# Performance work log

Hardware: AMD Instinct MI355X
Metric: run time of the kernel (lower is better)

Reference implementation:

```python
import jax, jax.numpy as jnp
import numpy as np

B = 65536
IN1, IN2 = 384, 128
GRU1, GRU2, NLEVELS = 384, 16, 256


def gru_step(x, h, kernel, rkernel, bias):
    """Single Keras GRU (reset_after=True) step. Gate order: z, r, h.
    kernel: [in, 3u], rkernel: [u, 3u], bias: [2, 3u] (input bias, recurrent bias)."""
    u = h.shape[-1]
    xi = x @ kernel + bias[0]          # [B, 3u]
    hr = h @ rkernel + bias[1]         # [B, 3u]
    xz, xr, xh = xi[:, :u], xi[:, u:2 * u], xi[:, 2 * u:]
    hz, hrr, hh = hr[:, :u], hr[:, u:2 * u], hr[:, 2 * u:]
    z = jax.nn.sigmoid(xz + hz)
    r = jax.nn.sigmoid(xr + hrr)
    hcand = jnp.tanh(xh + r * hh)
    return z * h + (1.0 - z) * hcand


def setup_inputs() -> dict:
    key = jax.random.key(0)
    ks = jax.random.split(key, 14)
    s = lambda fan: 1.0 / np.sqrt(fan)
    return {
        "x1": jax.random.normal(ks[0], (B, IN1), jnp.float32),
        "x2": jax.random.normal(ks[1], (B, IN2), jnp.float32),
        "gru1_kernel": jax.random.normal(ks[2], (IN1 + IN2, 3 * GRU1), jnp.float32) * s(IN1 + IN2),
        "gru1_rkernel": jax.random.normal(ks[3], (GRU1, 3 * GRU1), jnp.float32) * s(GRU1),
        "gru1_bias": jax.random.normal(ks[4], (2, 3 * GRU1), jnp.float32) * 0.01,
        "gru2_kernel": jax.random.normal(ks[5], (GRU1, 3 * GRU2), jnp.float32) * s(GRU1),
        "gru2_rkernel": jax.random.normal(ks[6], (GRU2, 3 * GRU2), jnp.float32) * s(GRU2),
        "gru2_bias": jax.random.normal(ks[7], (2, 3 * GRU2), jnp.float32) * 0.01,
        "fc_w1": jax.random.normal(ks[8], (GRU2, NLEVELS), jnp.float32) * s(GRU2),
        "fc_b1": jax.random.normal(ks[9], (NLEVELS,), jnp.float32) * 0.01,
        "fc_w2": jax.random.normal(ks[10], (GRU2, NLEVELS), jnp.float32) * s(GRU2),
        "fc_b2": jax.random.normal(ks[11], (NLEVELS,), jnp.float32) * 0.01,
        "fc_g1": jax.random.normal(ks[12], (NLEVELS,), jnp.float32),
        "fc_g2": jax.random.normal(ks[13], (NLEVELS,), jnp.float32),
    }


def reference(x1, x2, gru1_kernel, gru1_rkernel, gru1_bias,
              gru2_kernel, gru2_rkernel, gru2_bias,
              fc_w1, fc_b1, fc_w2, fc_b2, fc_g1, fc_g2):
    e = jnp.concatenate([x1, x2], axis=-1)                      # [B, 512]
    h1 = gru_step(e, jnp.zeros((e.shape[0], GRU1), e.dtype),
                  gru1_kernel, gru1_rkernel, gru1_bias)         # [B, 384]
    h2 = gru_step(h1, jnp.zeros((e.shape[0], GRU2), e.dtype),
                  gru2_kernel, gru2_rkernel, gru2_bias)         # [B, 16]
    # DualFC (LPCNet): weighted sum of two tanh branches
    d = fc_g1 * jnp.tanh(h2 @ fc_w1 + fc_b1) + fc_g2 * jnp.tanh(h2 @ fc_w2 + fc_b2)
    return jax.nn.softmax(d, axis=-1)                           # [B, 256]
```

## Files before the change

### kernel.cpp

```cpp
#include <hip/hip_runtime.h>

typedef unsigned short u16;
typedef unsigned int   u32;
typedef float f32x4 __attribute__((ext_vector_type(4)));
typedef short s16x8 __attribute__((ext_vector_type(8)));

#define NB    65536
#define K1    512
#define N1    1152
#define G1D   384
#define K2    384
#define G2D   16
#define NL    256

__device__ inline u16 f2bf(float f) {
  u32 u = __float_as_uint(f);
  u += 0x7fffu + ((u >> 16) & 1u);
  return (u16)(u >> 16);
}
__device__ inline float bf2f(u16 h) { return __uint_as_float(((u32)h) << 16); }
__device__ inline float sigmoidf_(float x) { return 1.0f / (1.0f + __expf(-x)); }
__device__ inline float tanhf_(float x) {
  float e = __expf(2.0f * fabsf(x));
  float t = 1.0f - 2.0f / (e + 1.0f);
  return copysignf(t, x);
}

__device__ inline void gld16(const u16* g, u16* l) {
  __builtin_amdgcn_global_load_lds(
      (const __attribute__((address_space(1))) void*)g,
      (__attribute__((address_space(3))) void*)l, 16, 0, 0);
}

__global__ void prep_a(const float* __restrict__ x1, const float* __restrict__ x2,
                       u16* __restrict__ Abf) {
  int t = blockIdx.x * 256 + threadIdx.x;
  int i = t * 8;
  int row = i >> 9, col = i & 511;
  const float* src = (col < 384) ? (x1 + row * 384 + col) : (x2 + row * 128 + (col - 384));
  float4 v0 = ((const float4*)src)[0];
  float4 v1 = ((const float4*)src)[1];
  union { uint4 v; u16 u[8]; } o;
  o.u[0] = f2bf(v0.x); o.u[1] = f2bf(v0.y); o.u[2] = f2bf(v0.z); o.u[3] = f2bf(v0.w);
  o.u[4] = f2bf(v1.x); o.u[5] = f2bf(v1.y); o.u[6] = f2bf(v1.z); o.u[7] = f2bf(v1.w);
  *(uint4*)(Abf + i) = o.v;
}

__global__ __launch_bounds__(256) void prep_wt1(const float* __restrict__ w,
                                                u16* __restrict__ wt) {
  __shared__ float tile[64][65];
  const int nt = blockIdx.x * 64;
  const int ktb = blockIdx.y * 64;
  const int tr = threadIdx.x >> 4;
  const int tc = (threadIdx.x & 15) * 4;
#pragma unroll
  for (int p = 0; p < 4; p++) {
    int k = ktb + p * 16 + tr;
    float4 v = *(const float4*)(w + (long)k * N1 + nt + tc);
    tile[p * 16 + tr][tc + 0] = v.x;
    tile[p * 16 + tr][tc + 1] = v.y;
    tile[p * 16 + tr][tc + 2] = v.z;
    tile[p * 16 + tr][tc + 3] = v.w;
  }
  __syncthreads();
  const int nl = threadIdx.x >> 3;
  const int kc = (threadIdx.x & 7) * 8;
#pragma unroll
  for (int p = 0; p < 2; p++) {
    int n = nl + p * 32;
    int c = nt + n;
    int g = c / 384;
    int urem = c - g * 384;
    int ut = urem >> 4, u16c = urem & 15;
    int k0 = ktb + kc;
    int kt = k0 >> 5, qd = (k0 >> 3) & 3;
    union { uint4 v; u16 u[8]; } o;
#pragma unroll
    for (int j = 0; j < 8; j++) o.u[j] = f2bf(tile[kc + j][n]);
    long off = ((long)((g * 24 + ut) * 16 + kt) * 64 + qd * 16 + u16c) * 8;
    *(uint4*)(wt + off) = o.v;
  }
}

__global__ void prep_wt(const float* __restrict__ w, u16* __restrict__ wt, int K, int N) {
  int n = blockIdx.x;
  int k0 = threadIdx.x * 8;
  if (k0 >= K) return;
  union { uint4 v; u16 u[8]; } o;
#pragma unroll
  for (int j = 0; j < 8; j++) o.u[j] = f2bf(w[(k0 + j) * N + n]);
  *(uint4*)(wt + n * K + k0) = o.v;
}

__global__ __launch_bounds__(256, 2) void gemm1gate(const u16* __restrict__ A,
                                                    const u16* __restrict__ Bf,
                                                    const float* __restrict__ bias,
                                                    u16* __restrict__ H1) {
  __shared__ u16 As[4][128 * 32];
  const int tid = threadIdx.x;
  const int wave = tid >> 6, lane = tid & 63;
  const int quad = lane >> 4, l16 = lane & 15;

  const int id = blockIdx.x;
  const int xcd = id & 7;
  const int s = id >> 3;
  const int sd6 = s / 6;
  const int ublk = s - sd6 * 6;
  const int mbase = (xcd * 64 + sd6) * 128;
  const int ucbase = ublk * 64;

  const int wm = (wave & 1) * 64, wu = (wave >> 1) * 32;
  const int ut0 = ublk * 4 + (wave >> 1) * 2;

  f32x4 acc[3][4][2];
#pragma unroll
  for (int g = 0; g < 3; g++)
#pragma unroll
    for (int i = 0; i < 4; i++)
#pragma unroll
      for (int j = 0; j < 2; j++)
#pragma unroll
        for (int r = 0; r < 4; r++) acc[g][i][j][r] = 0.0f;

  const int r0 = tid >> 2;
  const int kcg = ((tid & 3) ^ ((r0 >> 1) & 3)) * 8;
  const u16* Aptr  = A + (long)(mbase + r0) * K1 + kcg;
  const u16* Aptr2 = Aptr + 64 * K1;
  const u16* Bl = Bf + lane * 8;

  int aoff[4];
#pragma unroll
  for (int i = 0; i < 4; i++) {
    int ra = wm + i * 16 + l16;
    aoff[i] = ra * 32 + ((quad ^ ((ra >> 1) & 3)) << 3);
  }

  s16x8 bn[3][2];
#pragma unroll
  for (int g = 0; g < 3; g++)
#pragma unroll
    for (int j = 0; j < 2; j++)
      bn[g][j] = *(const s16x8*)(Bl + (long)((g * 24 + ut0 + j) * 16 + 0) * 512);
  asm volatile("" ::: "memory");
  gld16(Aptr,       &As[0][tid * 8]);
  gld16(Aptr2,      &As[0][2048 + tid * 8]);
  gld16(Aptr + 32,  &As[1][tid * 8]);
  gld16(Aptr2 + 32, &As[1][2048 + tid * 8]);

#pragma unroll
  for (int t = 0; t < 16; ++t) {
    s16x8 bcur[3][2];
#pragma unroll
    for (int g = 0; g < 3; g++)
#pragma unroll
      for (int j = 0; j < 2; j++) bcur[g][j] = bn[g][j];

    if (t < 15) {
      const int tb = t + 1;
#pragma unroll
      for (int g = 0; g < 3; g++)
#pragma unroll
        for (int j = 0; j < 2; j++)
          bn[g][j] = *(const s16x8*)(Bl + (long)((g * 24 + ut0 + j) * 16 + tb) * 512);
    }
    asm volatile("" ::: "memory");
    if (t < 14) {
      const int ta = t + 2;
      gld16(Aptr  + ta * 32, &As[(t + 2) & 3][tid * 8]);
      gld16(Aptr2 + ta * 32, &As[(t + 2) & 3][2048 + tid * 8]);
    }
    if (t == 0)       asm volatile("s_waitcnt vmcnt(10)" ::: "memory");
    else if (t < 14)  asm volatile("s_waitcnt vmcnt(16)" ::: "memory");
    else if (t == 14) asm volatile("s_waitcnt vmcnt(14)" ::: "memory");
    else              asm volatile("s_waitcnt vmcnt(6)"  ::: "memory");
    __builtin_amdgcn_s_barrier();
    asm volatile("" ::: "memory");

    const u16* buf = &As[t & 3][0];
    s16x8 af[4];
#pragma unroll
    for (int i = 0; i < 4; i++) af[i] = *(const s16x8*)(buf + aoff[i]);

    __builtin_amdgcn_s_setprio(1);
#pragma unroll
    for (int g = 0; g < 3; g++) {
#pragma unroll
      for (int mi = 0; mi < 4; mi++) {
        acc[g][mi][0] = __builtin_amdgcn_mfma_f32_16x16x32_bf16(af[mi], bcur[g][0], acc[g][mi][0], 0, 0, 0);
        acc[g][mi][1] = __builtin_amdgcn_mfma_f32_16x16x32_bf16(af[mi], bcur[g][1], acc[g][mi][1], 0, 0, 0);
      }
    }
    __builtin_amdgcn_s_setprio(0);
  }

#pragma unroll
  for (int j = 0; j < 2; j++) {
    int u = ucbase + wu + j * 16 + l16;
    float bz = bias[u] + bias[1152 + u];
    float br = bias[384 + u] + bias[1536 + u];
    float bh0 = bias[768 + u];
    float bh1 = bias[1920 + u];
#pragma unroll
    for (int mi = 0; mi < 4; mi++) {
#pragma unroll
      for (int rr = 0; rr < 4; rr++) {
        int row = mbase + wm + mi * 16 + quad * 4 + rr;
        float z  = sigmoidf_(acc[0][mi][j][rr] + bz);
        float rg = sigmoidf_(acc[1][mi][j][rr] + br);
        float hc = tanhf_(acc[2][mi][j][rr] + bh0 + rg * bh1);
        H1[(long)row * G1D + u] = f2bf((1.0f - z) * hc);
      }
    }
  }
}

__global__ __launch_bounds__(256) void gemm2fc(const u16* __restrict__ H1b,
                                               const u16* __restrict__ W2t,
                                               const float* __restrict__ bias2,
                                               const float* __restrict__ w1,
                                               const float* __restrict__ fb1,
                                               const float* __restrict__ w2,
                                               const float* __restrict__ fb2,
                                               const float* __restrict__ g1,
                                               const float* __restrict__ g2,
                                               float* __restrict__ out) {
  __shared__ u16 As[128 * 32];
  __shared__ u16 Bs[48 * 32];
  __shared__ float h2s[128 * 17];
  const int tid = threadIdx.x;
  const int wave = tid >> 6, lane = tid & 63;
  const int quad = lane >> 4, l16 = lane & 15;
  const int mbase = blockIdx.x * 128;

  f32x4 acc[2][3];
#pragma unroll
  for (int i = 0; i < 2; i++)
#pragma unroll
    for (int j = 0; j < 3; j++)
#pragma unroll
      for (int r = 0; r < 4; r++) acc[i][j][r] = 0.0f;

  const int r0 = tid >> 2, kc = (tid & 3) * 8;
  const u16* Aptr = H1b + (long)(mbase + r0) * K2 + kc;

  for (int k0 = 0; k0 < K2; k0 += 32) {
    uint4 a0 = *(const uint4*)(Aptr + k0);
    uint4 a1 = *(const uint4*)(Aptr + 64 * K2 + k0);
    uint4 bv;
    if (tid < 192) bv = *(const uint4*)(W2t + r0 * K2 + k0 + kc);
    __syncthreads();
    *(uint4*)(&As[r0 * 32 + kc]) = a0;
    *(uint4*)(&As[(64 + r0) * 32 + kc]) = a1;
    if (tid < 192) *(uint4*)(&Bs[r0 * 32 + kc]) = bv;
    __syncthreads();
    s16x8 af[2], bfr[3];
#pragma unroll
    for (int mi = 0; mi < 2; mi++)
      af[mi] = *(const s16x8*)(&As[(wave * 32 + mi * 16 + l16) * 32 + quad * 8]);
#pragma unroll
    for (int ni = 0; ni < 3; ni++)
      bfr[ni] = *(const s16x8*)(&Bs[(ni * 16 + l16) * 32 + quad * 8]);
#pragma unroll
    for (int mi = 0; mi < 2; mi++)
#pragma unroll
      for (int ni = 0; ni < 3; ni++)
        acc[mi][ni] = __builtin_amdgcn_mfma_f32_16x16x32_bf16(af[mi], bfr[ni], acc[mi][ni], 0, 0, 0);
  }

  {
    const int u = l16;
    const float b0z = bias2[u],      b1z = bias2[48 + u];
    const float b0r = bias2[16 + u], b1r = bias2[64 + u];
    const float b0h = bias2[32 + u], b1h = bias2[80 + u];
#pragma unroll
    for (int mi = 0; mi < 2; mi++) {
#pragma unroll
      for (int rr = 0; rr < 4; rr++) {
        int row_l = wave * 32 + mi * 16 + quad * 4 + rr;
        float z  = sigmoidf_(acc[mi][0][rr] + b0z + b1z);
        float rg = sigmoidf_(acc[mi][1][rr] + b0r + b1r);
        float hc = tanhf_(acc[mi][2][rr] + b0h + rg * b1h);
        h2s[row_l * 17 + u] = (1.0f - z) * hc;
      }
    }
  }
  __syncthreads();

#pragma unroll 1
  for (int r = 0; r < 32; r++) {
    int row_l = wave * 32 + r;
    float h[16];
#pragma unroll
    for (int uu = 0; uu < 16; uu++) h[uu] = h2s[row_l * 17 + uu];
    float e[4];
    float mx = -1e30f;
#pragma unroll
    for (int i = 0; i < 4; i++) {
      int c = i * 64 + lane;
      float a1 = fb1[c], a2 = fb2[c];
#pragma unroll
      for (int uu = 0; uu < 16; uu++) {
        a1 = fmaf(h[uu], w1[uu * 256 + c], a1);
        a2 = fmaf(h[uu], w2[uu * 256 + c], a2);
      }
      float d = g1[c] * tanhf_(a1) + g2[c] * tanhf_(a2);
      e[i] = d;
      mx = fmaxf(mx, d);
    }
#pragma unroll
    for (int off = 32; off >= 1; off >>= 1) mx = fmaxf(mx, __shfl_xor(mx, off, 64));
    float sum = 0.0f;
#pragma unroll
    for (int i = 0; i < 4; i++) { e[i] = __expf(e[i] - mx); sum += e[i]; }
#pragma unroll
    for (int off = 32; off >= 1; off >>= 1) sum += __shfl_xor(sum, off, 64);
    float inv = 1.0f / sum;
    float* orow = out + (long)(mbase + row_l) * NL;
#pragma unroll
    for (int i = 0; i < 4; i++) orow[i * 64 + lane] = e[i] * inv;
  }
}

extern "C" void kernel_launch(void* const* d_in, const int* in_sizes, int n_in,
                              void* d_out, int out_size, void* d_ws, size_t ws_size,
                              hipStream_t stream) {
  const float* x1   = (const float*)d_in[0];
  const float* x2   = (const float*)d_in[1];
  const float* w1k  = (const float*)d_in[2];
  const float* b1g  = (const float*)d_in[4];
  const float* w2k  = (const float*)d_in[5];
  const float* b2g  = (const float*)d_in[7];
  const float* fcw1 = (const float*)d_in[8];
  const float* fcb1 = (const float*)d_in[9];
  const float* fcw2 = (const float*)d_in[10];
  const float* fcb2 = (const float*)d_in[11];
  const float* fcg1 = (const float*)d_in[12];
  const float* fcg2 = (const float*)d_in[13];
  float* out = (float*)d_out;

  char* ws = (char*)d_ws;
  u16* Abf = (u16*)(ws + 0);
  u16* W1t = (u16*)(ws + 67108864);
  u16* H1  = (u16*)(ws + 68288512);
  u16* W2t = (u16*)(ws + 118620160);

  hipLaunchKernelGGL(prep_a, dim3(16384), dim3(256), 0, stream, x1, x2, Abf);
  hipLaunchKernelGGL(prep_wt1, dim3(18, 8), dim3(256), 0, stream, w1k, W1t);
  hipLaunchKernelGGL(prep_wt, dim3(48), dim3(64), 0, stream, w2k, W2t, 384, 48);
  hipLaunchKernelGGL(gemm1gate, dim3(3072), dim3(256), 0, stream, Abf, W1t, b1g, H1);
  hipLaunchKernelGGL(gemm2fc, dim3(512), dim3(256), 0, stream, H1, W2t, b2g,
                     fcw1, fcb1, fcw2, fcb2, fcg1, fcg2, out);
}
```

Baseline: 364.9 us.

## Halve gemm1gate tile width to double occupancy and block count

```diff
diff --git a/kernel.cpp b/kernel.cpp
--- a/kernel.cpp
+++ b/kernel.cpp
@@ -92,7 +92,7 @@
   *(uint4*)(wt + n * K + k0) = o.v;
 }
 
-__global__ __launch_bounds__(256, 2) void gemm1gate(const u16* __restrict__ A,
+__global__ __launch_bounds__(256, 4) void gemm1gate(const u16* __restrict__ A,
                                                     const u16* __restrict__ Bf,
                                                     const float* __restrict__ bias,
                                                     u16* __restrict__ H1) {
@@ -104,23 +104,22 @@
   const int id = blockIdx.x;
   const int xcd = id & 7;
   const int s = id >> 3;
-  const int sd6 = s / 6;
-  const int ublk = s - sd6 * 6;
-  const int mbase = (xcd * 64 + sd6) * 128;
-  const int ucbase = ublk * 64;
-
-  const int wm = (wave & 1) * 64, wu = (wave >> 1) * 32;
-  const int ut0 = ublk * 4 + (wave >> 1) * 2;
-
-  f32x4 acc[3][4][2];
+  const int sd = s / 12;
+  const int ublk = s - sd * 12;
+  const int mbase = (xcd * 64 + sd) * 128;
+  const int ucbase = ublk * 32;
+
+  const int wm = (wave & 1) * 64;
+  const int wuidx = wave >> 1;
+  const int ut0 = ublk * 2 + wuidx;
+
+  f32x4 acc[3][4];
 #pragma unroll
   for (int g = 0; g < 3; g++)
 #pragma unroll
     for (int i = 0; i < 4; i++)
 #pragma unroll
-      for (int j = 0; j < 2; j++)
-#pragma unroll
-        for (int r = 0; r < 4; r++) acc[g][i][j][r] = 0.0f;
+      for (int r = 0; r < 4; r++) acc[g][i][r] = 0.0f;
 
   const int r0 = tid >> 2;
   const int kcg = ((tid & 3) ^ ((r0 >> 1) & 3)) * 8;
@@ -135,12 +134,10 @@
     aoff[i] = ra * 32 + ((quad ^ ((ra >> 1) & 3)) << 3);
   }
 
-  s16x8 bn[3][2];
+  s16x8 bn[3];
 #pragma unroll
   for (int g = 0; g < 3; g++)
-#pragma unroll
-    for (int j = 0; j < 2; j++)
-      bn[g][j] = *(const s16x8*)(Bl + (long)((g * 24 + ut0 + j) * 16 + 0) * 512);
+    bn[g] = *(const s16x8*)(Bl + (long)((g * 24 + ut0) * 16 + 0) * 512);
   asm volatile("" ::: "memory");
   gld16(Aptr,       &As[0][tid * 8]);
   gld16(Aptr2,      &As[0][2048 + tid * 8]);
@@ -149,19 +146,15 @@
 
 #pragma unroll
   for (int t = 0; t < 16; ++t) {
-    s16x8 bcur[3][2];
-#pragma unroll
-    for (int g = 0; g < 3; g++)
-#pragma unroll
-      for (int j = 0; j < 2; j++) bcur[g][j] = bn[g][j];
+    s16x8 bcur[3];
+#pragma unroll
+    for (int g = 0; g < 3; g++) bcur[g] = bn[g];
 
     if (t < 15) {
       const int tb = t + 1;
 #pragma unroll
       for (int g = 0; g < 3; g++)
-#pragma unroll
-        for (int j = 0; j < 2; j++)
-          bn[g][j] = *(const s16x8*)(Bl + (long)((g * 24 + ut0 + j) * 16 + tb) * 512);
+        bn[g] = *(const s16x8*)(Bl + (long)((g * 24 + ut0) * 16 + tb) * 512);
     }
     asm volatile("" ::: "memory");
     if (t < 14) {
@@ -169,10 +162,9 @@
       gld16(Aptr  + ta * 32, &As[(t + 2) & 3][tid * 8]);
       gld16(Aptr2 + ta * 32, &As[(t + 2) & 3][2048 + tid * 8]);
     }
-    if (t == 0)       asm volatile("s_waitcnt vmcnt(10)" ::: "memory");
-    else if (t < 14)  asm volatile("s_waitcnt vmcnt(16)" ::: "memory");
-    else if (t == 14) asm volatile("s_waitcnt vmcnt(14)" ::: "memory");
-    else              asm volatile("s_waitcnt vmcnt(6)"  ::: "memory");
+    if (t < 14)       asm volatile("s_waitcnt vmcnt(7)" ::: "memory");
+    else if (t == 14) asm volatile("s_waitcnt vmcnt(5)" ::: "memory");
+    else              asm volatile("s_waitcnt vmcnt(0)" ::: "memory");
     __builtin_amdgcn_s_barrier();
     asm volatile("" ::: "memory");
 
@@ -186,16 +178,14 @@
     for (int g = 0; g < 3; g++) {
 #pragma unroll
       for (int mi = 0; mi < 4; mi++) {
-        acc[g][mi][0] = __builtin_amdgcn_mfma_f32_16x16x32_bf16(af[mi], bcur[g][0], acc[g][mi][0], 0, 0, 0);
-        acc[g][mi][1] = __builtin_amdgcn_mfma_f32_16x16x32_bf16(af[mi], bcur[g][1], acc[g][mi][1], 0, 0, 0);
+        acc[g][mi] = __builtin_amdgcn_mfma_f32_16x16x32_bf16(af[mi], bcur[g], acc[g][mi], 0, 0, 0);
       }
     }
     __builtin_amdgcn_s_setprio(0);
   }
 
-#pragma unroll
-  for (int j = 0; j < 2; j++) {
-    int u = ucbase + wu + j * 16 + l16;
+  {
+    int u = ucbase + wuidx * 16 + l16;
     float bz = bias[u] + bias[1152 + u];
     float br = bias[384 + u] + bias[1536 + u];
     float bh0 = bias[768 + u];
@@ -205,9 +195,9 @@
 #pragma unroll
       for (int rr = 0; rr < 4; rr++) {
         int row = mbase + wm + mi * 16 + quad * 4 + rr;
-        float z  = sigmoidf_(acc[0][mi][j][rr] + bz);
-        float rg = sigmoidf_(acc[1][mi][j][rr] + br);
-        float hc = tanhf_(acc[2][mi][j][rr] + bh0 + rg * bh1);
+        float z  = sigmoidf_(acc[0][mi][rr] + bz);
+        float rg = sigmoidf_(acc[1][mi][rr] + br);
+        float hc = tanhf_(acc[2][mi][rr] + bh0 + rg * bh1);
         H1[(long)row * G1D + u] = f2bf((1.0f - z) * hc);
       }
     }
@@ -347,7 +337,7 @@
   hipLaunchKernelGGL(prep_a, dim3(16384), dim3(256), 0, stream, x1, x2, Abf);
   hipLaunchKernelGGL(prep_wt1, dim3(18, 8), dim3(256), 0, stream, w1k, W1t);
   hipLaunchKernelGGL(prep_wt, dim3(48), dim3(64), 0, stream, w2k, W2t, 384, 48);
-  hipLaunchKernelGGL(gemm1gate, dim3(3072), dim3(256), 0, stream, Abf, W1t, b1g, H1);
+  hipLaunchKernelGGL(gemm1gate, dim3(6144), dim3(256), 0, stream, Abf, W1t, b1g, H1);
   hipLaunchKernelGGL(gemm2fc, dim3(512), dim3(256), 0, stream, H1, W2t, b2g,
                      fcw1, fcb1, fcw2, fcb2, fcg1, fcg2, out);
 }
```

Result: slower. 373.2 us (+2.3%).

## Retile GRU1 GEMM to 256-row blocks and merge weight prep kernels

Applied to the files above, without the earlier changes.

```diff
diff --git a/kernel.cpp b/kernel.cpp
--- a/kernel.cpp
+++ b/kernel.cpp
@@ -46,57 +46,61 @@
   *(uint4*)(Abf + i) = o.v;
 }
 
-__global__ __launch_bounds__(256) void prep_wt1(const float* __restrict__ w,
-                                                u16* __restrict__ wt) {
+__global__ __launch_bounds__(256) void prep_w(const float* __restrict__ w1k,
+                                              u16* __restrict__ W1t,
+                                              const float* __restrict__ w2k,
+                                              u16* __restrict__ W2t) {
   __shared__ float tile[64][65];
-  const int nt = blockIdx.x * 64;
-  const int ktb = blockIdx.y * 64;
-  const int tr = threadIdx.x >> 4;
-  const int tc = (threadIdx.x & 15) * 4;
-#pragma unroll
-  for (int p = 0; p < 4; p++) {
-    int k = ktb + p * 16 + tr;
-    float4 v = *(const float4*)(w + (long)k * N1 + nt + tc);
-    tile[p * 16 + tr][tc + 0] = v.x;
-    tile[p * 16 + tr][tc + 1] = v.y;
-    tile[p * 16 + tr][tc + 2] = v.z;
-    tile[p * 16 + tr][tc + 3] = v.w;
-  }
-  __syncthreads();
-  const int nl = threadIdx.x >> 3;
-  const int kc = (threadIdx.x & 7) * 8;
-#pragma unroll
-  for (int p = 0; p < 2; p++) {
-    int n = nl + p * 32;
-    int c = nt + n;
-    int g = c / 384;
-    int urem = c - g * 384;
-    int ut = urem >> 4, u16c = urem & 15;
-    int k0 = ktb + kc;
-    int kt = k0 >> 5, qd = (k0 >> 3) & 3;
-    union { uint4 v; u16 u[8]; } o;
-#pragma unroll
-    for (int j = 0; j < 8; j++) o.u[j] = f2bf(tile[kc + j][n]);
-    long off = ((long)((g * 24 + ut) * 16 + kt) * 64 + qd * 16 + u16c) * 8;
-    *(uint4*)(wt + off) = o.v;
-  }
-}
-
-__global__ void prep_wt(const float* __restrict__ w, u16* __restrict__ wt, int K, int N) {
-  int n = blockIdx.x;
-  int k0 = threadIdx.x * 8;
-  if (k0 >= K) return;
-  union { uint4 v; u16 u[8]; } o;
-#pragma unroll
-  for (int j = 0; j < 8; j++) o.u[j] = f2bf(w[(k0 + j) * N + n]);
-  *(uint4*)(wt + n * K + k0) = o.v;
+  const int id = blockIdx.x;
+  if (id < 144) {
+    const int nt = (id % 18) * 64;
+    const int ktb = (id / 18) * 64;
+    const int tr = threadIdx.x >> 4;
+    const int tc = (threadIdx.x & 15) * 4;
+#pragma unroll
+    for (int p = 0; p < 4; p++) {
+      int k = ktb + p * 16 + tr;
+      float4 v = *(const float4*)(w1k + (long)k * N1 + nt + tc);
+      tile[p * 16 + tr][tc + 0] = v.x;
+      tile[p * 16 + tr][tc + 1] = v.y;
+      tile[p * 16 + tr][tc + 2] = v.z;
+      tile[p * 16 + tr][tc + 3] = v.w;
+    }
+    __syncthreads();
+    const int nl = threadIdx.x >> 3;
+    const int kc = (threadIdx.x & 7) * 8;
+#pragma unroll
+    for (int p = 0; p < 2; p++) {
+      int n = nl + p * 32;
+      int c = nt + n;
+      int g = c / 384;
+      int urem = c - g * 384;
+      int ut = urem >> 4, u16c = urem & 15;
+      int k0 = ktb + kc;
+      int kt = k0 >> 5, qd = (k0 >> 3) & 3;
+      union { uint4 v; u16 u[8]; } o;
+#pragma unroll
+      for (int j = 0; j < 8; j++) o.u[j] = f2bf(tile[kc + j][n]);
+      long off = ((long)((g * 24 + ut) * 16 + kt) * 64 + qd * 16 + u16c) * 8;
+      *(uint4*)(W1t + off) = o.v;
+    }
+  } else {
+    const int n = id - 144;
+    if (threadIdx.x < 48) {
+      const int k0 = threadIdx.x * 8;
+      union { uint4 v; u16 u[8]; } o;
+#pragma unroll
+      for (int j = 0; j < 8; j++) o.u[j] = f2bf(w2k[(k0 + j) * 48 + n]);
+      *(uint4*)(W2t + n * K2 + k0) = o.v;
+    }
+  }
 }
 
 __global__ __launch_bounds__(256, 2) void gemm1gate(const u16* __restrict__ A,
                                                     const u16* __restrict__ Bf,
                                                     const float* __restrict__ bias,
                                                     u16* __restrict__ H1) {
-  __shared__ u16 As[4][128 * 32];
+  __shared__ u16 As[4][256 * 32];
   const int tid = threadIdx.x;
   const int wave = tid >> 6, lane = tid & 63;
   const int quad = lane >> 4, l16 = lane & 15;
@@ -104,13 +108,12 @@
   const int id = blockIdx.x;
   const int xcd = id & 7;
   const int s = id >> 3;
-  const int sd6 = s / 6;
-  const int ublk = s - sd6 * 6;
-  const int mbase = (xcd * 64 + sd6) * 128;
-  const int ucbase = ublk * 64;
-
-  const int wm = (wave & 1) * 64, wu = (wave >> 1) * 32;
-  const int ut0 = ublk * 4 + (wave >> 1) * 2;
+  const int sd = s / 12;
+  const int ublk = s - sd * 12;
+  const int mbase = (xcd * 32 + sd) * 256;
+  const int ucbase = ublk * 32;
+  const int wm = wave * 64;
+  const int ut0 = ublk * 2;
 
   f32x4 acc[3][4][2];
 #pragma unroll
@@ -124,8 +127,10 @@
 
   const int r0 = tid >> 2;
   const int kcg = ((tid & 3) ^ ((r0 >> 1) & 3)) * 8;
-  const u16* Aptr  = A + (long)(mbase + r0) * K1 + kcg;
-  const u16* Aptr2 = Aptr + 64 * K1;
+  const u16* Ap0 = A + (long)(mbase + r0) * K1 + kcg;
+  const u16* Ap1 = Ap0 + 64 * K1;
+  const u16* Ap2 = Ap0 + 128 * K1;
+  const u16* Ap3 = Ap0 + 192 * K1;
   const u16* Bl = Bf + lane * 8;
 
   int aoff[4];
@@ -135,17 +140,27 @@
     aoff[i] = ra * 32 + ((quad ^ ((ra >> 1) & 3)) << 3);
   }
 
+#define BLOAD(T, DST) do {                                                   \
+    _Pragma("unroll")                                                        \
+    for (int g_ = 0; g_ < 3; g_++)                                           \
+      _Pragma("unroll")                                                      \
+      for (int j_ = 0; j_ < 2; j_++)                                         \
+        DST[g_][j_] = *(const s16x8*)(Bl +                                   \
+            (long)((g_ * 24 + ut0 + j_) * 16 + (T)) * 512);                  \
+  } while (0)
+
+#define STAGEA(T, BUFI) do {                                                 \
+    gld16(Ap0 + (T) * 32, &As[BUFI][0 * 2048 + tid * 8]);                    \
+    gld16(Ap1 + (T) * 32, &As[BUFI][1 * 2048 + tid * 8]);                    \
+    gld16(Ap2 + (T) * 32, &As[BUFI][2 * 2048 + tid * 8]);                    \
+    gld16(Ap3 + (T) * 32, &As[BUFI][3 * 2048 + tid * 8]);                    \
+  } while (0)
+
   s16x8 bn[3][2];
-#pragma unroll
-  for (int g = 0; g < 3; g++)
-#pragma unroll
-    for (int j = 0; j < 2; j++)
-      bn[g][j] = *(const s16x8*)(Bl + (long)((g * 24 + ut0 + j) * 16 + 0) * 512);
+  BLOAD(0, bn);
   asm volatile("" ::: "memory");
-  gld16(Aptr,       &As[0][tid * 8]);
-  gld16(Aptr2,      &As[0][2048 + tid * 8]);
-  gld16(Aptr + 32,  &As[1][tid * 8]);
-  gld16(Aptr2 + 32, &As[1][2048 + tid * 8]);
+  STAGEA(0, 0);
+  STAGEA(1, 1);
 
 #pragma unroll
   for (int t = 0; t < 16; ++t) {
@@ -155,24 +170,12 @@
 #pragma unroll
       for (int j = 0; j < 2; j++) bcur[g][j] = bn[g][j];
 
-    if (t < 15) {
-      const int tb = t + 1;
-#pragma unroll
-      for (int g = 0; g < 3; g++)
-#pragma unroll
-        for (int j = 0; j < 2; j++)
-          bn[g][j] = *(const s16x8*)(Bl + (long)((g * 24 + ut0 + j) * 16 + tb) * 512);
-    }
+    if (t < 15) BLOAD(t + 1, bn);
     asm volatile("" ::: "memory");
-    if (t < 14) {
-      const int ta = t + 2;
-      gld16(Aptr  + ta * 32, &As[(t + 2) & 3][tid * 8]);
-      gld16(Aptr2 + ta * 32, &As[(t + 2) & 3][2048 + tid * 8]);
-    }
-    if (t == 0)       asm volatile("s_waitcnt vmcnt(10)" ::: "memory");
-    else if (t < 14)  asm volatile("s_waitcnt vmcnt(16)" ::: "memory");
-    else if (t == 14) asm volatile("s_waitcnt vmcnt(14)" ::: "memory");
-    else              asm volatile("s_waitcnt vmcnt(6)"  ::: "memory");
+    if (t < 14) STAGEA(t + 2, (t + 2) & 3);
+    if (t < 14)       asm volatile("s_waitcnt vmcnt(14)" ::: "memory");
+    else if (t == 14) asm volatile("s_waitcnt vmcnt(10)" ::: "memory");
+    else              asm volatile("s_waitcnt vmcnt(0)"  ::: "memory");
     __builtin_amdgcn_s_barrier();
     asm volatile("" ::: "memory");
 
@@ -192,10 +195,12 @@
     }
     __builtin_amdgcn_s_setprio(0);
   }
+#undef BLOAD
+#undef STAGEA
 
 #pragma unroll
   for (int j = 0; j < 2; j++) {
-    int u = ucbase + wu + j * 16 + l16;
+    int u = ucbase + j * 16 + l16;
     float bz = bias[u] + bias[1152 + u];
     float br = bias[384 + u] + bias[1536 + u];
     float bh0 = bias[768 + u];
@@ -345,8 +350,7 @@
   u16* W2t = (u16*)(ws + 118620160);
 
   hipLaunchKernelGGL(prep_a, dim3(16384), dim3(256), 0, stream, x1, x2, Abf);
-  hipLaunchKernelGGL(prep_wt1, dim3(18, 8), dim3(256), 0, stream, w1k, W1t);
-  hipLaunchKernelGGL(prep_wt, dim3(48), dim3(64), 0, stream, w2k, W2t, 384, 48);
+  hipLaunchKernelGGL(prep_w, dim3(192), dim3(256), 0, stream, w1k, W1t, w2k, W2t);
   hipLaunchKernelGGL(gemm1gate, dim3(3072), dim3(256), 0, stream, Abf, W1t, b1g, H1);
   hipLaunchKernelGGL(gemm2fc, dim3(512), dim3(256), 0, stream, H1, W2t, b2g,
                      fcw1, fcb1, fcw2, fcb2, fcg1, fcg2, out);
```

After: 369.8 us. No clear change (+1.3%).
